# Performance work log

Hardware: AMD Instinct MI355X
Metric: run time of the kernel (lower is better)

Reference implementation:

```python
import jax, jax.numpy as jnp
import numpy as np

D_MODEL = 1024
NUM_HEADS = 16
D_K = D_MODEL // NUM_HEADS
THETA = 10000.0
NEG_INF = -1e9


def _rope(x, positions):
    # x: [B, H, S, d_k]; rotate interleaved (even, odd) pairs as complex mult
    half = D_K // 2
    inv_freq = 1.0 / (THETA ** (jnp.arange(0, D_K, 2, dtype=jnp.float32) / D_K))  # [half]
    angles = positions.astype(jnp.float32)[:, None] * inv_freq  # [S, half]
    cos, sin = jnp.cos(angles), jnp.sin(angles)
    xe = x[..., 0::2]
    xo = x[..., 1::2]
    re = xe * cos - xo * sin
    ro = xe * sin + xo * cos
    return jnp.stack([re, ro], axis=-1).reshape(x.shape).astype(x.dtype)


def setup_inputs() -> dict:
    key = jax.random.key(0)
    ks = jax.random.split(key, 5)
    sigma = np.sqrt(2.0 / (D_MODEL + D_MODEL))
    x = jax.random.normal(ks[0], (2, 2048, D_MODEL), dtype=jnp.float32)
    mk = lambda k: (sigma * jax.random.normal(k, (D_MODEL, D_MODEL))).astype(jnp.float32)
    return {
        "x": x,
        "Wq": mk(ks[1]), "bq": jnp.zeros((D_MODEL,), jnp.float32),
        "Wk": mk(ks[2]), "bk": jnp.zeros((D_MODEL,), jnp.float32),
        "Wv": mk(ks[3]), "bv": jnp.zeros((D_MODEL,), jnp.float32),
        "Wo": mk(ks[4]), "bo": jnp.zeros((D_MODEL,), jnp.float32),
        "token_positions": jnp.arange(2048, dtype=jnp.int64) if jax.config.jax_enable_x64 else jnp.arange(2048, dtype=jnp.int32),
    }


def reference(x, Wq, bq, Wk, bk, Wv, bv, Wo, bo, token_positions):
    B, S, D = x.shape
    # Linear stores weight as [in, out] and computes x @ W.T + b
    Q = x @ Wq.T + bq
    K = x @ Wk.T + bk
    V = x @ Wv.T + bv
    def split_heads(t):  # [B,S,D] -> [B,H,S,d_k]
        return t.reshape(B, S, NUM_HEADS, D_K).transpose(0, 2, 1, 3)
    Q, K, V = split_heads(Q), split_heads(K), split_heads(V)
    # the torch forward always uses arange positions (it overwrites token_positions)
    pos = jnp.arange(S)
    Q = _rope(Q, pos)
    K = _rope(K, pos)
    scale = 1.0 / jnp.sqrt(jnp.float32(D_K))
    scores = jnp.einsum("bhqd,bhkd->bhqk", Q, K) * scale
    causal = jnp.tril(jnp.ones((S, S), dtype=bool))  # allowed where key <= query
    scores = jnp.where(causal, scores, NEG_INF)
    weights = jax.nn.softmax(scores, axis=-1)
    attn = jnp.einsum("bhqk,bhkd->bhqd", weights, V)  # [B,H,S,d_k]
    concat = attn.transpose(0, 2, 1, 3).reshape(B, S, D)
    return concat @ Wo.T + bo
```

## Files before the change

### kernel.cpp

```cpp
#include <hip/hip_runtime.h>
#include <hip/hip_bf16.h>
#include <math.h>

#define D_MODEL 1024
#define NH      16
#define DK      64
#define SEQ     2048
#define BATCH   2
#define RTOT    (BATCH*SEQ)

typedef __attribute__((ext_vector_type(8))) short bf16x8;
typedef __attribute__((ext_vector_type(4))) float f32x4;

__device__ __forceinline__ float bf2f(unsigned short u) {
    union { unsigned int i; float f; } v; v.i = ((unsigned int)u) << 16; return v.f;
}
__device__ __forceinline__ unsigned short f2bf(float f) {
    union { float f; unsigned int i; } v; v.f = f;
    unsigned int r = v.i + 0x7FFFu + ((v.i >> 16) & 1u);
    return (unsigned short)(r >> 16);
}
__device__ __forceinline__ unsigned short f2bf_hw(float f) {
    __hip_bfloat16 h = __float2bfloat16(f);
    union { __hip_bfloat16 h; unsigned short u; } v; v.h = h; return v.u;
}
__device__ __forceinline__ unsigned int pack2bf(float a, float b) {
    return (unsigned int)f2bf(a) | ((unsigned int)f2bf(b) << 16);
}

__device__ __forceinline__ void gload_lds16(const unsigned short* g,
                                            unsigned short* l) {
    __builtin_amdgcn_global_load_lds(
        (const __attribute__((address_space(1))) void*)g,
        (__attribute__((address_space(3))) void*)l, 16, 0, 0);
}

__device__ __forceinline__ void stage128x32(
    const unsigned short* __restrict__ src, int ldk,
    unsigned short* lds, int w, int lane)
{
    #pragma unroll
    for (int p = 0; p < 2; ++p) {
        const int ckb = (w * 2 + p) * 64;
        const int ck  = ckb + lane;
        const int row = ck >> 2;
        const int cs  = (ck & 3) ^ ((row >> 1) & 3);
        gload_lds16(src + (size_t)row * ldk + cs * 8, lds + (size_t)ckb * 8);
    }
}

__global__ __launch_bounds__(256) void prep(
    const float* __restrict__ X,  const float* __restrict__ Wq,
    const float* __restrict__ Wk, const float* __restrict__ Wv,
    const float* __restrict__ Wo,
    unsigned short* __restrict__ Xbf, unsigned short* __restrict__ Wqkvbf,
    unsigned short* __restrict__ Wobf, float2* __restrict__ rope)
{
    const int id = blockIdx.x * 256 + threadIdx.x;
    const float* src;
    unsigned short* dst;
    size_t off;
    if (id < 524288) {
        src = X; dst = Xbf; off = (size_t)id * 8;
    } else {
        const int j   = id - 524288;
        const int mat = j >> 17;
        off = (size_t)(j & 131071) * 8;
        src = (mat == 0) ? Wq : (mat == 1) ? Wk : (mat == 2) ? Wv : Wo;
        dst = (mat < 3) ? (Wqkvbf + (size_t)mat * 1048576) : Wobf;
    }
    const float4 a = *(const float4*)&src[off];
    const float4 b = *(const float4*)&src[off + 4];
    uint4 p;
    p.x = pack2bf(a.x, a.y); p.y = pack2bf(a.z, a.w);
    p.z = pack2bf(b.x, b.y); p.w = pack2bf(b.z, b.w);
    *(uint4*)&dst[off] = p;

    if (id < SEQ * 32) {
        const int s  = id >> 5;
        const int fi = id & 31;
        const float ang = (float)s * powf(10000.0f, -(float)(2 * fi) * (1.0f / 64.0f));
        float c, sn;
        sincosf(ang, &c, &sn);
        rope[id] = make_float2(c, sn);
    }
}

__global__ __launch_bounds__(256) void gemm_qkv_bf(
    const unsigned short* __restrict__ Xb, const unsigned short* __restrict__ Wall,
    const float* __restrict__ bq, const float* __restrict__ bk,
    const float* __restrict__ bv, const float2* __restrict__ rope,
    unsigned short* __restrict__ Qw, unsigned short* __restrict__ Kw,
    unsigned short* __restrict__ Vw)
{
    __shared__ unsigned short Ab[2][128 * 32];
    __shared__ unsigned short Bb[2][128 * 32];

    const int t    = threadIdx.x;
    const int ct   = blockIdx.x;
    const int mat  = ct >> 3;
    const int col0 = (ct & 7) * 128;
    const int row0 = blockIdx.y * 128;

    const unsigned short* W = Wall + (size_t)mat * 1048576;
    const float* bias = (mat == 0) ? bq : (mat == 1) ? bk : bv;
    unsigned short* Y = (mat == 0) ? Qw : (mat == 1) ? Kw : Vw;

    const int lane = t & 63;
    const int wave = t >> 6;
    const int wm   = (wave >> 1) * 64;
    const int wn   = (wave & 1) * 64;
    const int l15  = lane & 15;
    const int quad = lane >> 4;

    f32x4 acc[4][4];
    #pragma unroll
    for (int i = 0; i < 4; ++i)
        #pragma unroll
        for (int j = 0; j < 4; ++j) acc[i][j] = (f32x4){0.f, 0.f, 0.f, 0.f};

    const unsigned short* Asrc = &Xb[(size_t)row0 * D_MODEL];
    const unsigned short* Bsrc = &W[(size_t)col0 * D_MODEL];

    stage128x32(Asrc, D_MODEL, Ab[0], wave, lane);
    stage128x32(Bsrc, D_MODEL, Bb[0], wave, lane);
    __syncthreads();

    for (int kt = 0; kt < 32; ++kt) {
        const int cur = kt & 1;
        if (kt + 1 < 32) {
            stage128x32(Asrc + (kt + 1) * 32, D_MODEL, Ab[cur ^ 1], wave, lane);
            stage128x32(Bsrc + (kt + 1) * 32, D_MODEL, Bb[cur ^ 1], wave, lane);
        }
        bf16x8 af[4], bfr[4];
        #pragma unroll
        for (int i = 0; i < 4; ++i) {
            const int r = wm + i * 16 + l15;
            af[i] = *(const bf16x8*)&Ab[cur][r * 32 + ((quad ^ ((r >> 1) & 3)) * 8)];
        }
        #pragma unroll
        for (int j = 0; j < 4; ++j) {
            const int r = wn + j * 16 + l15;
            bfr[j] = *(const bf16x8*)&Bb[cur][r * 32 + ((quad ^ ((r >> 1) & 3)) * 8)];
        }
        #pragma unroll
        for (int i = 0; i < 4; ++i)
            #pragma unroll
            for (int j = 0; j < 4; ++j)
                acc[i][j] = __builtin_amdgcn_mfma_f32_16x16x32_bf16(
                    af[i], bfr[j], acc[i][j], 0, 0, 0);
        __syncthreads();
    }

    #pragma unroll
    for (int i = 0; i < 4; ++i) {
        #pragma unroll
        for (int j = 0; j < 4; ++j) {
            const int cl = col0 + wn + j * 16 + l15;
            const int h  = cl >> 6;
            const int dk = cl & 63;
            const int fi = (cl & 63) >> 1;
            const float bsv = bias[cl];
            #pragma unroll
            for (int r = 0; r < 4; ++r) {
                const int row = row0 + wm + i * 16 + quad * 4 + r;
                const int s   = row & (SEQ - 1);
                const int b   = row >> 11;
                float v = acc[i][j][r] + bsv;
                if (mat == 0) v *= 0.125f;
                if (mat < 2) {
                    const float2 cs = rope[s * 32 + fi];
                    const float p = __shfl_xor(v, 1, 64);
                    v = v * cs.x + ((l15 & 1) ? -p * cs.y : p * cs.y);
                }
                Y[((size_t)(b * NH + h) * SEQ + s) * DK + dk] = f2bf(v);
            }
        }
    }
}

__global__ __launch_bounds__(256) void gemm_qkv_f32(
    const float* __restrict__ X,
    const float* __restrict__ Wq, const float* __restrict__ bq,
    const float* __restrict__ Wk, const float* __restrict__ bk,
    const float* __restrict__ Wv, const float* __restrict__ bv,
    unsigned short* __restrict__ Qw, unsigned short* __restrict__ Kw,
    unsigned short* __restrict__ Vw)
{
    __shared__ unsigned short Ab[128 * 40];
    __shared__ unsigned short Bb[128 * 40];

    const int t    = threadIdx.x;
    const int ct   = blockIdx.x;
    const int mat  = ct >> 3;
    const int col0 = (ct & 7) * 128;
    const int row0 = blockIdx.y * 128;

    const float* W    = (mat == 0) ? Wq : (mat == 1) ? Wk : Wv;
    const float* bias = (mat == 0) ? bq : (mat == 1) ? bk : bv;
    unsigned short* Y = (mat == 0) ? Qw : (mat == 1) ? Kw : Vw;

    const int srow  = t >> 1;
    const int skseg = (t & 1) * 16;

    const int lane = t & 63;
    const int wave = t >> 6;
    const int wm   = (wave >> 1) * 64;
    const int wn   = (wave & 1) * 64;
    const int l15  = lane & 15;
    const int quad = lane >> 4;

    f32x4 acc[4][4];
    #pragma unroll
    for (int i = 0; i < 4; ++i)
        #pragma unroll
        for (int j = 0; j < 4; ++j) acc[i][j] = (f32x4){0.f, 0.f, 0.f, 0.f};

    for (int k0 = 0; k0 < D_MODEL; k0 += 32) {
        const float* xs = &X[(size_t)(row0 + srow) * D_MODEL + k0 + skseg];
        const float* ws = &W[(size_t)(col0 + srow) * D_MODEL + k0 + skseg];
        float4 x0 = *(const float4*)&xs[0],  x1 = *(const float4*)&xs[4];
        float4 x2 = *(const float4*)&xs[8],  x3 = *(const float4*)&xs[12];
        float4 w0 = *(const float4*)&ws[0],  w1 = *(const float4*)&ws[4];
        float4 w2 = *(const float4*)&ws[8],  w3 = *(const float4*)&ws[12];
        uint4 pa0, pa1, pb0, pb1;
        pa0.x = pack2bf(x0.x, x0.y); pa0.y = pack2bf(x0.z, x0.w);
        pa0.z = pack2bf(x1.x, x1.y); pa0.w = pack2bf(x1.z, x1.w);
        pa1.x = pack2bf(x2.x, x2.y); pa1.y = pack2bf(x2.z, x2.w);
        pa1.z = pack2bf(x3.x, x3.y); pa1.w = pack2bf(x3.z, x3.w);
        pb0.x = pack2bf(w0.x, w0.y); pb0.y = pack2bf(w0.z, w0.w);
        pb0.z = pack2bf(w1.x, w1.y); pb0.w = pack2bf(w1.z, w1.w);
        pb1.x = pack2bf(w2.x, w2.y); pb1.y = pack2bf(w2.z, w2.w);
        pb1.z = pack2bf(w3.x, w3.y); pb1.w = pack2bf(w3.z, w3.w);
        __syncthreads();
        *(uint4*)&Ab[srow * 40 + skseg]     = pa0;
        *(uint4*)&Ab[srow * 40 + skseg + 8] = pa1;
        *(uint4*)&Bb[srow * 40 + skseg]     = pb0;
        *(uint4*)&Bb[srow * 40 + skseg + 8] = pb1;
        __syncthreads();

        bf16x8 af[4], bfr[4];
        #pragma unroll
        for (int i = 0; i < 4; ++i)
            af[i] = *(const bf16x8*)&Ab[(wm + i * 16 + l15) * 40 + quad * 8];
        #pragma unroll
        for (int j = 0; j < 4; ++j)
            bfr[j] = *(const bf16x8*)&Bb[(wn + j * 16 + l15) * 40 + quad * 8];
        #pragma unroll
        for (int i = 0; i < 4; ++i)
            #pragma unroll
            for (int j = 0; j < 4; ++j)
                acc[i][j] = __builtin_amdgcn_mfma_f32_16x16x32_bf16(
                    af[i], bfr[j], acc[i][j], 0, 0, 0);
    }

    float invj[4];
    #pragma unroll
    for (int j = 0; j < 4; ++j) {
        const int cl = col0 + wn + j * 16 + l15;
        const int fi = (cl & 63) >> 1;
        invj[j] = powf(10000.0f, -(float)(2 * fi) * (1.0f / 64.0f));
    }
    #pragma unroll
    for (int i = 0; i < 4; ++i) {
        #pragma unroll
        for (int j = 0; j < 4; ++j) {
            const int cl = col0 + wn + j * 16 + l15;
            const int h  = cl >> 6;
            const int dk = cl & 63;
            const float bsv = bias[cl];
            #pragma unroll
            for (int r = 0; r < 4; ++r) {
                const int row = row0 + wm + i * 16 + quad * 4 + r;
                const int s   = row & (SEQ - 1);
                const int b   = row >> 11;
                float v = acc[i][j][r] + bsv;
                if (mat == 0) v *= 0.125f;
                if (mat < 2) {
                    float c, sn;
                    sincosf((float)s * invj[j], &c, &sn);
                    const float p = __shfl_xor(v, 1, 64);
                    v = v * c + ((l15 & 1) ? -p * sn : p * sn);
                }
                Y[((size_t)(b * NH + h) * SEQ + s) * DK + dk] = f2bf(v);
            }
        }
    }
}

__global__ __launch_bounds__(256) void gemm_out_bf(
    const unsigned short* __restrict__ A, const unsigned short* __restrict__ W,
    const float* __restrict__ bias, float* __restrict__ out)
{
    __shared__ unsigned short Ab[2][128 * 32];
    __shared__ unsigned short Bb[2][128 * 32];

    const int t    = threadIdx.x;
    const int col0 = blockIdx.x * 128;
    const int row0 = blockIdx.y * 128;

    const int lane = t & 63;
    const int wave = t >> 6;
    const int wm   = (wave >> 1) * 64;
    const int wn   = (wave & 1) * 64;
    const int l15  = lane & 15;
    const int quad = lane >> 4;

    f32x4 acc[4][4];
    #pragma unroll
    for (int i = 0; i < 4; ++i)
        #pragma unroll
        for (int j = 0; j < 4; ++j) acc[i][j] = (f32x4){0.f, 0.f, 0.f, 0.f};

    const unsigned short* Asrc = &A[(size_t)row0 * D_MODEL];
    const unsigned short* Bsrc = &W[(size_t)col0 * D_MODEL];

    stage128x32(Asrc, D_MODEL, Ab[0], wave, lane);
    stage128x32(Bsrc, D_MODEL, Bb[0], wave, lane);
    __syncthreads();

    for (int kt = 0; kt < 32; ++kt) {
        const int cur = kt & 1;
        if (kt + 1 < 32) {
            stage128x32(Asrc + (kt + 1) * 32, D_MODEL, Ab[cur ^ 1], wave, lane);
            stage128x32(Bsrc + (kt + 1) * 32, D_MODEL, Bb[cur ^ 1], wave, lane);
        }
        bf16x8 af[4], bfr[4];
        #pragma unroll
        for (int i = 0; i < 4; ++i) {
            const int r = wm + i * 16 + l15;
            af[i] = *(const bf16x8*)&Ab[cur][r * 32 + ((quad ^ ((r >> 1) & 3)) * 8)];
        }
        #pragma unroll
        for (int j = 0; j < 4; ++j) {
            const int r = wn + j * 16 + l15;
            bfr[j] = *(const bf16x8*)&Bb[cur][r * 32 + ((quad ^ ((r >> 1) & 3)) * 8)];
        }
        #pragma unroll
        for (int i = 0; i < 4; ++i)
            #pragma unroll
            for (int j = 0; j < 4; ++j)
                acc[i][j] = __builtin_amdgcn_mfma_f32_16x16x32_bf16(
                    af[i], bfr[j], acc[i][j], 0, 0, 0);
        __syncthreads();
    }

    #pragma unroll
    for (int i = 0; i < 4; ++i) {
        #pragma unroll
        for (int j = 0; j < 4; ++j) {
            const int col = col0 + wn + j * 16 + l15;
            const float bsv = bias[col];
            #pragma unroll
            for (int r = 0; r < 4; ++r) {
                const int row = row0 + wm + i * 16 + quad * 4 + r;
                out[(size_t)row * D_MODEL + col] = acc[i][j][r] + bsv;
            }
        }
    }
}

__global__ __launch_bounds__(256) void gemm_out_f32(
    const unsigned short* __restrict__ A, const float* __restrict__ W,
    const float* __restrict__ bias, float* __restrict__ out)
{
    __shared__ unsigned short Ab[128 * 40];
    __shared__ unsigned short Bb[128 * 40];

    const int t    = threadIdx.x;
    const int col0 = blockIdx.x * 128;
    const int row0 = blockIdx.y * 128;

    const int srow  = t >> 1;
    const int skseg = (t & 1) * 16;

    const int lane = t & 63;
    const int wave = t >> 6;
    const int wm   = (wave >> 1) * 64;
    const int wn   = (wave & 1) * 64;
    const int l15  = lane & 15;
    const int quad = lane >> 4;

    f32x4 acc[4][4];
    #pragma unroll
    for (int i = 0; i < 4; ++i)
        #pragma unroll
        for (int j = 0; j < 4; ++j) acc[i][j] = (f32x4){0.f, 0.f, 0.f, 0.f};

    for (int k0 = 0; k0 < D_MODEL; k0 += 32) {
        const unsigned short* as = &A[(size_t)(row0 + srow) * D_MODEL + k0 + skseg];
        uint4 ua0 = *(const uint4*)&as[0];
        uint4 ua1 = *(const uint4*)&as[8];
        const float* ws = &W[(size_t)(col0 + srow) * D_MODEL + k0 + skseg];
        float4 w0 = *(const float4*)&ws[0],  w1 = *(const float4*)&ws[4];
        float4 w2 = *(const float4*)&ws[8],  w3 = *(const float4*)&ws[12];
        uint4 pb0, pb1;
        pb0.x = pack2bf(w0.x, w0.y); pb0.y = pack2bf(w0.z, w0.w);
        pb0.z = pack2bf(w1.x, w1.y); pb0.w = pack2bf(w1.z, w1.w);
        pb1.x = pack2bf(w2.x, w2.y); pb1.y = pack2bf(w2.z, w2.w);
        pb1.z = pack2bf(w3.x, w3.y); pb1.w = pack2bf(w3.z, w3.w);
        __syncthreads();
        *(uint4*)&Ab[srow * 40 + skseg]     = ua0;
        *(uint4*)&Ab[srow * 40 + skseg + 8] = ua1;
        *(uint4*)&Bb[srow * 40 + skseg]     = pb0;
        *(uint4*)&Bb[srow * 40 + skseg + 8] = pb1;
        __syncthreads();

        bf16x8 af[4], bfr[4];
        #pragma unroll
        for (int i = 0; i < 4; ++i)
            af[i] = *(const bf16x8*)&Ab[(wm + i * 16 + l15) * 40 + quad * 8];
        #pragma unroll
        for (int j = 0; j < 4; ++j)
            bfr[j] = *(const bf16x8*)&Bb[(wn + j * 16 + l15) * 40 + quad * 8];
        #pragma unroll
        for (int i = 0; i < 4; ++i)
            #pragma unroll
            for (int j = 0; j < 4; ++j)
                acc[i][j] = __builtin_amdgcn_mfma_f32_16x16x32_bf16(
                    af[i], bfr[j], acc[i][j], 0, 0, 0);
    }

    #pragma unroll
    for (int i = 0; i < 4; ++i) {
        #pragma unroll
        for (int j = 0; j < 4; ++j) {
            const int col = col0 + wn + j * 16 + l15;
            const float bsv = bias[col];
            #pragma unroll
            for (int r = 0; r < 4; ++r) {
                const int row = row0 + wm + i * 16 + quad * 4 + r;
                out[(size_t)row * D_MODEL + col] = acc[i][j][r] + bsv;
            }
        }
    }
}

#define DEFER_THR 16.0f

__device__ __forceinline__ void attn_tile_proc(
    const f32x4* sc, const bf16x8* vf,
    float& m, f32x4& lsum, f32x4* od,
    bool diag, int w, int l15, int quad)
{
    float s[4][4];
    float pmax = -3.0e38f;
    #pragma unroll
    for (int kc = 0; kc < 4; ++kc) {
        const int kbase = 8 * quad + 4 * (kc & 1) + 32 * (kc >> 1);
        #pragma unroll
        for (int r = 0; r < 4; ++r) {
            float v = sc[kc][r];
            if (diag && (kbase + r > w * 16 + l15)) v = -1.0e9f;
            s[kc][r] = v;
            pmax = fmaxf(pmax, v);
        }
    }
    pmax = fmaxf(pmax, __shfl_xor(pmax, 16, 64));
    pmax = fmaxf(pmax, __shfl_xor(pmax, 32, 64));

    if (!__all(pmax <= m + DEFER_THR)) {
        const float mnew  = fmaxf(m, pmax);
        const float alpha = __expf(m - mnew);
        m = mnew;
        #pragma unroll
        for (int r = 0; r < 4; ++r) {
            const float ar = __shfl(alpha, quad * 20 + r, 64);
            lsum[r] *= ar;
            #pragma unroll
            for (int dt = 0; dt < 4; ++dt) od[dt][r] *= ar;
        }
    }

    bf16x8 pa0, pa1;
    #pragma unroll
    for (int kc = 0; kc < 4; ++kc) {
        #pragma unroll
        for (int r = 0; r < 4; ++r) {
            const unsigned short b = f2bf_hw(__expf(s[kc][r] - m));
            const int e = 4 * (kc & 1) + r;
            if ((kc >> 1) == 0) pa0[e] = (short)b;
            else                pa1[e] = (short)b;
        }
    }

    bf16x8 ones;
    #pragma unroll
    for (int e = 0; e < 8; ++e) ones[e] = (short)0x3F80;

    __builtin_amdgcn_s_setprio(1);
    f32x4 rs = (f32x4){0.f, 0.f, 0.f, 0.f};
    rs = __builtin_amdgcn_mfma_f32_16x16x32_bf16(pa0, ones, rs, 0, 0, 0);
    rs = __builtin_amdgcn_mfma_f32_16x16x32_bf16(pa1, ones, rs, 0, 0, 0);
    #pragma unroll
    for (int dt = 0; dt < 4; ++dt) {
        od[dt] = __builtin_amdgcn_mfma_f32_16x16x32_bf16(pa0, vf[dt * 2],     od[dt], 0, 0, 0);
        od[dt] = __builtin_amdgcn_mfma_f32_16x16x32_bf16(pa1, vf[dt * 2 + 1], od[dt], 0, 0, 0);
    }
    __builtin_amdgcn_s_setprio(0);

    #pragma unroll
    for (int r = 0; r < 4; ++r) lsum[r] += rs[r];
}

__global__ __launch_bounds__(256) void attn_kernel(
    const unsigned short* __restrict__ Q, const unsigned short* __restrict__ K,
    const unsigned short* __restrict__ V, unsigned short* __restrict__ Out)
{
    __shared__ unsigned short Ks[2][64 * 72];
    __shared__ unsigned short Vt[2][64 * 72];

    const int qtA = blockIdx.x;
    const int qtB = (SEQ / 64 - 1) - qtA;
    const int bh  = blockIdx.y;
    const unsigned short* Qb = Q + (size_t)bh * SEQ * DK;
    const unsigned short* Kb = K + (size_t)bh * SEQ * DK;
    const unsigned short* Vb = V + (size_t)bh * SEQ * DK;

    const int t    = threadIdx.x;
    const int lane = t & 63;
    const int w    = t >> 6;
    const int l15  = lane & 15;
    const int quad = lane >> 4;

    const int qrowA = qtA * 64 + w * 16 + l15;
    const int qrowB = qtB * 64 + w * 16 + l15;
    bf16x8 qa0 = *(const bf16x8*)&Qb[(size_t)qrowA * DK + quad * 8];
    bf16x8 qa1 = *(const bf16x8*)&Qb[(size_t)qrowA * DK + 32 + quad * 8];
    bf16x8 qb0 = *(const bf16x8*)&Qb[(size_t)qrowB * DK + quad * 8];
    bf16x8 qb1 = *(const bf16x8*)&Qb[(size_t)qrowB * DK + 32 + quad * 8];

    f32x4 odA[4], odB[4];
    f32x4 lsA = (f32x4){0.f, 0.f, 0.f, 0.f};
    f32x4 lsB = (f32x4){0.f, 0.f, 0.f, 0.f};
    float mA = -3.0e38f, mB = -3.0e38f;
    #pragma unroll
    for (int r = 0; r < 4; ++r) {
        odA[r] = (f32x4){0.f, 0.f, 0.f, 0.f};
        odB[r] = (f32x4){0.f, 0.f, 0.f, 0.f};
    }

    const int tk = t >> 3;
    const int tc = t & 7;

    const int kp0 = tk ^ (tc * 8);
    const int kp1 = (32 + tk) ^ (tc * 8);
    const int ksw = (tk >> 3) & 3;
    const int kc0 = ((tc & 4) | ((tc & 3) ^ ksw)) * 8;

    bf16x8 kv0 = *(const bf16x8*)&Kb[((size_t)tk) * DK + tc * 8];
    bf16x8 kv1 = *(const bf16x8*)&Kb[((size_t)(32 + tk)) * DK + tc * 8];
    bf16x8 vv0 = *(const bf16x8*)&Vb[((size_t)tk) * DK + tc * 8];
    bf16x8 vv1 = *(const bf16x8*)&Vb[((size_t)(32 + tk)) * DK + tc * 8];

    *(bf16x8*)&Ks[0][tk * 72 + kc0]        = kv0;
    *(bf16x8*)&Ks[0][(32 + tk) * 72 + kc0] = kv1;
    #pragma unroll
    for (int e = 0; e < 8; ++e) {
        Vt[0][(tc * 8 + e) * 72 + kp0] = (unsigned short)vv0[e];
        Vt[0][(tc * 8 + e) * 72 + kp1] = (unsigned short)vv1[e];
    }
    kv0 = *(const bf16x8*)&Kb[((size_t)(64 + tk)) * DK + tc * 8];
    kv1 = *(const bf16x8*)&Kb[((size_t)(64 + 32 + tk)) * DK + tc * 8];
    vv0 = *(const bf16x8*)&Vb[((size_t)(64 + tk)) * DK + tc * 8];
    vv1 = *(const bf16x8*)&Vb[((size_t)(64 + 32 + tk)) * DK + tc * 8];
    __syncthreads();

    for (int j = 0; j <= qtB; ++j) {
        const int cur = j & 1;

        if (j < qtB) {
            *(bf16x8*)&Ks[cur ^ 1][tk * 72 + kc0]        = kv0;
            *(bf16x8*)&Ks[cur ^ 1][(32 + tk) * 72 + kc0] = kv1;
            #pragma unroll
            for (int e = 0; e < 8; ++e) {
                Vt[cur ^ 1][(tc * 8 + e) * 72 + kp0] = (unsigned short)vv0[e];
                Vt[cur ^ 1][(tc * 8 + e) * 72 + kp1] = (unsigned short)vv1[e];
            }
        }
        if (j + 2 <= qtB) {
            const size_t nb = (size_t)((j + 2) * 64);
            kv0 = *(const bf16x8*)&Kb[(nb + tk) * DK + tc * 8];
            kv1 = *(const bf16x8*)&Kb[(nb + 32 + tk) * DK + tc * 8];
            vv0 = *(const bf16x8*)&Vb[(nb + tk) * DK + tc * 8];
            vv1 = *(const bf16x8*)&Vb[(nb + 32 + tk) * DK + tc * 8];
        }

        const bool doA = (j <= qtA);

        bf16x8 kf[8];
        #pragma unroll
        for (int kc = 0; kc < 4; ++kc) {
            const int kr = ((l15 >> 2) << 3) + ((kc & 1) << 2)
                         + ((kc >> 1) << 5) + (l15 & 3);
            const int cs = (quad ^ ((kr >> 3) & 3)) * 8;
            kf[kc * 2]     = *(const bf16x8*)&Ks[cur][kr * 72 + cs];
            kf[kc * 2 + 1] = *(const bf16x8*)&Ks[cur][kr * 72 + 32 + cs];
        }

        f32x4 scA[4], scB[4];
        __builtin_amdgcn_s_setprio(1);
        #pragma unroll
        for (int kc = 0; kc < 4; ++kc) {
            f32x4 z = (f32x4){0.f, 0.f, 0.f, 0.f};
            z = __builtin_amdgcn_mfma_f32_16x16x32_bf16(kf[kc * 2],     qb0, z, 0, 0, 0);
            z = __builtin_amdgcn_mfma_f32_16x16x32_bf16(kf[kc * 2 + 1], qb1, z, 0, 0, 0);
            scB[kc] = z;
        }
        if (doA) {
            #pragma unroll
            for (int kc = 0; kc < 4; ++kc) {
                f32x4 z = (f32x4){0.f, 0.f, 0.f, 0.f};
                z = __builtin_amdgcn_mfma_f32_16x16x32_bf16(kf[kc * 2],     qa0, z, 0, 0, 0);
                z = __builtin_amdgcn_mfma_f32_16x16x32_bf16(kf[kc * 2 + 1], qa1, z, 0, 0, 0);
                scA[kc] = z;
            }
        }
        __builtin_amdgcn_s_setprio(0);

        bf16x8 vf[8];
        #pragma unroll
        for (int dt = 0; dt < 4; ++dt) {
            const int d  = dt * 16 + l15;
            const int sw = d & 0x38;
            vf[dt * 2]     = *(const bf16x8*)&Vt[cur][d * 72 + ((quad * 8) ^ sw)];
            vf[dt * 2 + 1] = *(const bf16x8*)&Vt[cur][d * 72 + ((32 + quad * 8) ^ sw)];
        }

        if (doA)
            attn_tile_proc(scA, vf, mA, lsA, odA, (j == qtA), w, l15, quad);
        attn_tile_proc(scB, vf, mB, lsB, odB, (j == qtB), w, l15, quad);

        __syncthreads();
    }

    const int b = bh >> 4;
    const int h = bh & 15;
    #pragma unroll
    for (int r = 0; r < 4; ++r) {
        const float rlA = 1.0f / lsA[r];
        const float rlB = 1.0f / lsB[r];
        const int qA = qtA * 64 + w * 16 + quad * 4 + r;
        const int qB = qtB * 64 + w * 16 + quad * 4 + r;
        #pragma unroll
        for (int dt = 0; dt < 4; ++dt) {
            Out[((size_t)(b * SEQ + qA)) * D_MODEL + h * DK + dt * 16 + l15] =
                f2bf(odA[dt][r] * rlA);
            Out[((size_t)(b * SEQ + qB)) * D_MODEL + h * DK + dt * 16 + l15] =
                f2bf(odB[dt][r] * rlB);
        }
    }
}

extern "C" void kernel_launch(void* const* d_in, const int* in_sizes, int n_in,
                              void* d_out, int out_size, void* d_ws, size_t ws_size,
                              hipStream_t stream) {
    const float* x  = (const float*)d_in[0];
    const float* Wq = (const float*)d_in[1];
    const float* bq = (const float*)d_in[2];
    const float* Wk = (const float*)d_in[3];
    const float* bk = (const float*)d_in[4];
    const float* Wv = (const float*)d_in[5];
    const float* bv = (const float*)d_in[6];
    const float* Wo = (const float*)d_in[7];
    const float* bo = (const float*)d_in[8];

    const size_t E = (size_t)RTOT * D_MODEL;
    float* out = (float*)d_out;
    dim3 blk(256);

    const size_t WS_NEED = (4 * E + 4 * (size_t)D_MODEL * D_MODEL) * 2
                         + (size_t)SEQ * 32 * sizeof(float2);

    unsigned short* Qws = (unsigned short*)d_ws;
    unsigned short* Kws = Qws + E;
    unsigned short* Vws = Kws + E;
    unsigned short* AXs = Vws + E;

    if (ws_size >= WS_NEED) {
        unsigned short* Wqkv = AXs + E;
        unsigned short* Wobf = Wqkv + (size_t)3 * D_MODEL * D_MODEL;
        float2*         rope = (float2*)(Wobf + (size_t)D_MODEL * D_MODEL);

        prep<<<4096, blk, 0, stream>>>(x, Wq, Wk, Wv, Wo, AXs, Wqkv, Wobf, rope);

        dim3 gq(24, RTOT / 128);
        gemm_qkv_bf<<<gq, blk, 0, stream>>>(AXs, Wqkv, bq, bk, bv, rope,
                                            Qws, Kws, Vws);

        dim3 ga(SEQ / 128, BATCH * NH);
        attn_kernel<<<ga, blk, 0, stream>>>(Qws, Kws, Vws, AXs);

        dim3 go(D_MODEL / 128, RTOT / 128);
        gemm_out_bf<<<go, blk, 0, stream>>>(AXs, Wobf, bo, out);
    } else {
        dim3 gq(24, RTOT / 128);
        gemm_qkv_f32<<<gq, blk, 0, stream>>>(x, Wq, bq, Wk, bk, Wv, bv,
                                             Qws, Kws, Vws);

        dim3 ga(SEQ / 128, BATCH * NH);
        attn_kernel<<<ga, blk, 0, stream>>>(Qws, Kws, Vws, AXs);

        dim3 go(D_MODEL / 128, RTOT / 128);
        gemm_out_f32<<<go, blk, 0, stream>>>(AXs, Wo, bo, out);
    }
}
```

Measured before the change: 212.1 us.

## Split paired query tiles across separate wavefronts in 512-thread attention blocks

The attention kernel now launches 512 threads per block. Waves 0-3 handle the low query tile and waves 4-7 the mirrored high query tile, where before each wave processed both tiles serially. K/V tile loading is split across twice as many threads, and register pressure per wave drops because each wave keeps only one set of accumulators. The risk is that the waves on the short tile sit idle at the barriers while the long tile finishes, and the larger block may lower how many blocks fit per CU.

```diff
diff --git a/kernel.cpp b/kernel.cpp
--- a/kernel.cpp
+++ b/kernel.cpp
@@ -441,7 +441,7 @@
 __device__ __forceinline__ void attn_tile_proc(
     const f32x4* sc, const bf16x8* vf,
     float& m, f32x4& lsum, f32x4* od,
-    bool diag, int w, int l15, int quad)
+    bool diag, int wq, int l15, int quad)
 {
     float s[4][4];
     float pmax = -3.0e38f;
@@ -451,7 +451,7 @@
         #pragma unroll
         for (int r = 0; r < 4; ++r) {
             float v = sc[kc][r];
-            if (diag && (kbase + r > w * 16 + l15)) v = -1.0e9f;
+            if (diag && (kbase + r > wq * 16 + l15)) v = -1.0e9f;
             s[kc][r] = v;
             pmax = fmaxf(pmax, v);
         }
@@ -503,7 +503,7 @@
     for (int r = 0; r < 4; ++r) lsum[r] += rs[r];
 }
 
-__global__ __launch_bounds__(256) void attn_kernel(
+__global__ __launch_bounds__(512) void attn_kernel(
     const unsigned short* __restrict__ Q, const unsigned short* __restrict__ K,
     const unsigned short* __restrict__ V, unsigned short* __restrict__ Out)
 {
@@ -520,116 +520,87 @@
     const int t    = threadIdx.x;
     const int lane = t & 63;
     const int w    = t >> 6;
+    const int wq   = w & 3;
+    const int qt   = (w < 4) ? qtA : qtB;
     const int l15  = lane & 15;
     const int quad = lane >> 4;
 
-    const int qrowA = qtA * 64 + w * 16 + l15;
-    const int qrowB = qtB * 64 + w * 16 + l15;
-    bf16x8 qa0 = *(const bf16x8*)&Qb[(size_t)qrowA * DK + quad * 8];
-    bf16x8 qa1 = *(const bf16x8*)&Qb[(size_t)qrowA * DK + 32 + quad * 8];
-    bf16x8 qb0 = *(const bf16x8*)&Qb[(size_t)qrowB * DK + quad * 8];
-    bf16x8 qb1 = *(const bf16x8*)&Qb[(size_t)qrowB * DK + 32 + quad * 8];
-
-    f32x4 odA[4], odB[4];
-    f32x4 lsA = (f32x4){0.f, 0.f, 0.f, 0.f};
-    f32x4 lsB = (f32x4){0.f, 0.f, 0.f, 0.f};
-    float mA = -3.0e38f, mB = -3.0e38f;
-    #pragma unroll
-    for (int r = 0; r < 4; ++r) {
-        odA[r] = (f32x4){0.f, 0.f, 0.f, 0.f};
-        odB[r] = (f32x4){0.f, 0.f, 0.f, 0.f};
-    }
+    const int qrow = qt * 64 + wq * 16 + l15;
+    bf16x8 q0 = *(const bf16x8*)&Qb[(size_t)qrow * DK + quad * 8];
+    bf16x8 q1 = *(const bf16x8*)&Qb[(size_t)qrow * DK + 32 + quad * 8];
+
+    f32x4 od[4];
+    f32x4 ls = (f32x4){0.f, 0.f, 0.f, 0.f};
+    float m = -3.0e38f;
+    #pragma unroll
+    for (int r = 0; r < 4; ++r) od[r] = (f32x4){0.f, 0.f, 0.f, 0.f};
 
     const int tk = t >> 3;
     const int tc = t & 7;
 
     const int kp0 = tk ^ (tc * 8);
-    const int kp1 = (32 + tk) ^ (tc * 8);
     const int ksw = (tk >> 3) & 3;
     const int kc0 = ((tc & 4) | ((tc & 3) ^ ksw)) * 8;
 
     bf16x8 kv0 = *(const bf16x8*)&Kb[((size_t)tk) * DK + tc * 8];
-    bf16x8 kv1 = *(const bf16x8*)&Kb[((size_t)(32 + tk)) * DK + tc * 8];
     bf16x8 vv0 = *(const bf16x8*)&Vb[((size_t)tk) * DK + tc * 8];
-    bf16x8 vv1 = *(const bf16x8*)&Vb[((size_t)(32 + tk)) * DK + tc * 8];
-
-    *(bf16x8*)&Ks[0][tk * 72 + kc0]        = kv0;
-    *(bf16x8*)&Ks[0][(32 + tk) * 72 + kc0] = kv1;
-    #pragma unroll
-    for (int e = 0; e < 8; ++e) {
+
+    *(bf16x8*)&Ks[0][tk * 72 + kc0] = kv0;
+    #pragma unroll
+    for (int e = 0; e < 8; ++e)
         Vt[0][(tc * 8 + e) * 72 + kp0] = (unsigned short)vv0[e];
-        Vt[0][(tc * 8 + e) * 72 + kp1] = (unsigned short)vv1[e];
-    }
     kv0 = *(const bf16x8*)&Kb[((size_t)(64 + tk)) * DK + tc * 8];
-    kv1 = *(const bf16x8*)&Kb[((size_t)(64 + 32 + tk)) * DK + tc * 8];
     vv0 = *(const bf16x8*)&Vb[((size_t)(64 + tk)) * DK + tc * 8];
-    vv1 = *(const bf16x8*)&Vb[((size_t)(64 + 32 + tk)) * DK + tc * 8];
     __syncthreads();
 
     for (int j = 0; j <= qtB; ++j) {
         const int cur = j & 1;
 
         if (j < qtB) {
-            *(bf16x8*)&Ks[cur ^ 1][tk * 72 + kc0]        = kv0;
-            *(bf16x8*)&Ks[cur ^ 1][(32 + tk) * 72 + kc0] = kv1;
-            #pragma unroll
-            for (int e = 0; e < 8; ++e) {
+            *(bf16x8*)&Ks[cur ^ 1][tk * 72 + kc0] = kv0;
+            #pragma unroll
+            for (int e = 0; e < 8; ++e)
                 Vt[cur ^ 1][(tc * 8 + e) * 72 + kp0] = (unsigned short)vv0[e];
-                Vt[cur ^ 1][(tc * 8 + e) * 72 + kp1] = (unsigned short)vv1[e];
-            }
         }
         if (j + 2 <= qtB) {
             const size_t nb = (size_t)((j + 2) * 64);
             kv0 = *(const bf16x8*)&Kb[(nb + tk) * DK + tc * 8];
-            kv1 = *(const bf16x8*)&Kb[(nb + 32 + tk) * DK + tc * 8];
             vv0 = *(const bf16x8*)&Vb[(nb + tk) * DK + tc * 8];
-            vv1 = *(const bf16x8*)&Vb[(nb + 32 + tk) * DK + tc * 8];
-        }
-
-        const bool doA = (j <= qtA);
-
-        bf16x8 kf[8];
-        #pragma unroll
-        for (int kc = 0; kc < 4; ++kc) {
-            const int kr = ((l15 >> 2) << 3) + ((kc & 1) << 2)
-                         + ((kc >> 1) << 5) + (l15 & 3);
-            const int cs = (quad ^ ((kr >> 3) & 3)) * 8;
-            kf[kc * 2]     = *(const bf16x8*)&Ks[cur][kr * 72 + cs];
-            kf[kc * 2 + 1] = *(const bf16x8*)&Ks[cur][kr * 72 + 32 + cs];
-        }
-
-        f32x4 scA[4], scB[4];
-        __builtin_amdgcn_s_setprio(1);
-        #pragma unroll
-        for (int kc = 0; kc < 4; ++kc) {
-            f32x4 z = (f32x4){0.f, 0.f, 0.f, 0.f};
-            z = __builtin_amdgcn_mfma_f32_16x16x32_bf16(kf[kc * 2],     qb0, z, 0, 0, 0);
-            z = __builtin_amdgcn_mfma_f32_16x16x32_bf16(kf[kc * 2 + 1], qb1, z, 0, 0, 0);
-            scB[kc] = z;
-        }
-        if (doA) {
+        }
+
+        if (j <= qt) {
+            bf16x8 kf[8];
+            #pragma unroll
+            for (int kc = 0; kc < 4; ++kc) {
+                const int kr = ((l15 >> 2) << 3) + ((kc & 1) << 2)
+                             + ((kc >> 1) << 5) + (l15 & 3);
+                const int cs = (quad ^ ((kr >> 3) & 3)) * 8;
+                kf[kc * 2]     = *(const bf16x8*)&Ks[cur][kr * 72 + cs];
+                kf[kc * 2 + 1] = *(const bf16x8*)&Ks[cur][kr * 72 + 32 + cs];
+            }
+
+            f32x4 sc[4];
+            __builtin_amdgcn_s_setprio(1);
             #pragma unroll
             for (int kc = 0; kc < 4; ++kc) {
                 f32x4 z = (f32x4){0.f, 0.f, 0.f, 0.f};
-                z = __builtin_amdgcn_mfma_f32_16x16x32_bf16(kf[kc * 2],     qa0, z, 0, 0, 0);
-                z = __builtin_amdgcn_mfma_f32_16x16x32_bf16(kf[kc * 2 + 1], qa1, z, 0, 0, 0);
-                scA[kc] = z;
+                z = __builtin_amdgcn_mfma_f32_16x16x32_bf16(kf[kc * 2],     q0, z, 0, 0, 0);
+                z = __builtin_amdgcn_mfma_f32_16x16x32_bf16(kf[kc * 2 + 1], q1, z, 0, 0, 0);
+                sc[kc] = z;
             }
-        }
-        __builtin_amdgcn_s_setprio(0);
-
-        bf16x8 vf[8];
-        #pragma unroll
-        for (int dt = 0; dt < 4; ++dt) {
-            const int d  = dt * 16 + l15;
-            const int sw = d & 0x38;
-            vf[dt * 2]     = *(const bf16x8*)&Vt[cur][d * 72 + ((quad * 8) ^ sw)];
-            vf[dt * 2 + 1] = *(const bf16x8*)&Vt[cur][d * 72 + ((32 + quad * 8) ^ sw)];
-        }
-
-        if (doA)
-            attn_tile_proc(scA, vf, mA, lsA, odA, (j == qtA), w, l15, quad);
-        attn_tile_proc(scB, vf, mB, lsB, odB, (j == qtB), w, l15, quad);
+            __builtin_amdgcn_s_setprio(0);
+
+            bf16x8 vf[8];
+            #pragma unroll
+            for (int dt = 0; dt < 4; ++dt) {
+                const int d  = dt * 16 + l15;
+                const int sw = d & 0x38;
+                vf[dt * 2]     = *(const bf16x8*)&Vt[cur][d * 72 + ((quad * 8) ^ sw)];
+                vf[dt * 2 + 1] = *(const bf16x8*)&Vt[cur][d * 72 + ((32 + quad * 8) ^ sw)];
+            }
+
+            attn_tile_proc(sc, vf, m, ls, od, (j == qt), wq, l15, quad);
+        }
 
         __syncthreads();
     }
@@ -638,17 +609,12 @@
     const int h = bh & 15;
     #pragma unroll
     for (int r = 0; r < 4; ++r) {
-        const float rlA = 1.0f / lsA[r];
-        const float rlB = 1.0f / lsB[r];
-        const int qA = qtA * 64 + w * 16 + quad * 4 + r;
-        const int qB = qtB * 64 + w * 16 + quad * 4 + r;
-        #pragma unroll
-        for (int dt = 0; dt < 4; ++dt) {
-            Out[((size_t)(b * SEQ + qA)) * D_MODEL + h * DK + dt * 16 + l15] =
-                f2bf(odA[dt][r] * rlA);
-            Out[((size_t)(b * SEQ + qB)) * D_MODEL + h * DK + dt * 16 + l15] =
-                f2bf(odB[dt][r] * rlB);
-        }
+        const float rl = 1.0f / ls[r];
+        const int q = qt * 64 + wq * 16 + quad * 4 + r;
+        #pragma unroll
+        for (int dt = 0; dt < 4; ++dt)
+            Out[((size_t)(b * SEQ + q)) * D_MODEL + h * DK + dt * 16 + l15] =
+                f2bf(od[dt][r] * rl);
     }
 }
 
@@ -689,7 +655,7 @@
                                             Qws, Kws, Vws);
 
         dim3 ga(SEQ / 128, BATCH * NH);
-        attn_kernel<<<ga, blk, 0, stream>>>(Qws, Kws, Vws, AXs);
+        attn_kernel<<<ga, dim3(512), 0, stream>>>(Qws, Kws, Vws, AXs);
 
         dim3 go(D_MODEL / 128, RTOT / 128);
         gemm_out_bf<<<go, blk, 0, stream>>>(AXs, Wobf, bo, out);
@@ -699,7 +665,7 @@
                                              Qws, Kws, Vws);
 
         dim3 ga(SEQ / 128, BATCH * NH);
-        attn_kernel<<<ga, blk, 0, stream>>>(Qws, Kws, Vws, AXs);
+        attn_kernel<<<ga, dim3(512), 0, stream>>>(Qws, Kws, Vws, AXs);
 
         dim3 go(D_MODEL / 128, RTOT / 128);
         gemm_out_f32<<<go, blk, 0, stream>>>(AXs, Wo, bo, out);
```

New measurement: 210.2 us. No clear change (-0.9%).
